# Kernel tuning notes

Hardware: AMD Instinct MI355X
Metric: run time of the kernel (lower is better)

## Reference

```python
import jax, jax.numpy as jnp
import numpy as np

TOP_K = 2


def setup_inputs() -> dict:
    key = jax.random.key(0)
    k1, k2 = jax.random.split(key)
    hidden_states = jax.random.normal(k1, (4, 8192, 4096), dtype=jnp.float32)
    weight = jax.random.normal(k2, (64, 4096), dtype=jnp.float32) * 0.02
    return {"hidden_states": hidden_states, "weight": weight}


def reference(hidden_states, weight):
    bsz, seq_len, h = hidden_states.shape
    x = hidden_states.reshape(-1, h)                      # [T, h]
    logits = jnp.einsum('th,eh->te', x, weight)           # [T, E] router logits
    scores = jax.nn.softmax(logits, axis=-1)
    topk_weight, topk_idx = jax.lax.top_k(scores, TOP_K)  # [T, k] each
    # norm_topk_prob is False in the module, so no renormalization.
    return topk_idx, topk_weight
```

## Files before the change

kernel.cpp:

```cpp
#include <hip/hip_runtime.h>
#include <math.h>


#define BK 64

__device__ __forceinline__ void gl_lds16(const float* g, float* l) {
  __builtin_amdgcn_global_load_lds(
      (const __attribute__((address_space(1))) unsigned int*)g,
      (__attribute__((address_space(3))) unsigned int*)l,
      16, 0, 0);
}

__global__ __launch_bounds__(256)
void moe_gate(const float* __restrict__ X, const float* __restrict__ W,
              float* __restrict__ out, int T) {
  __shared__ float smem[8192];
  float* sx = smem;
  float* sw = smem + 4096;

  const int t    = threadIdx.x;
  const int lane = t & 63;
  const int wave = t >> 6;
  const int tr   = t & 15;
  const int tc   = t >> 4;
  const long tok0 = (long)blockIdx.x * 64;

  const float* xg[4];
  const float* wg[4];
  float* ldx[4];
  float* ldw[4];
  {
    const int rl = lane >> 4;
    const int c4 = lane & 15;
    #pragma unroll
    for (int i = 0; i < 4; ++i) {
      const int r  = wave * 16 + i * 4 + rl;
      const int sz = (wave * 4 + i) & 15;
      const int gc = c4 ^ sz;
      xg[i] = X + (tok0 + r) * 4096 + gc * 4;
      wg[i] = W + (long)r * 4096 + gc * 4;
      ldx[i] = sx + (wave * 16 + i * 4) * 64;
      ldw[i] = sw + (wave * 16 + i * 4) * 64;
    }
  }

  float acc[4][4];
  #pragma unroll
  for (int i = 0; i < 4; ++i)
    #pragma unroll
    for (int j = 0; j < 4; ++j) acc[i][j] = 0.f;

  for (int k0 = 0; k0 < 4096; k0 += BK) {
    #pragma unroll
    for (int i = 0; i < 4; ++i) {
      gl_lds16(xg[i] + k0, ldx[i]);
      gl_lds16(wg[i] + k0, ldw[i]);
    }
    __syncthreads();

    float cacc[4][4];
    #pragma unroll
    for (int i = 0; i < 4; ++i)
      #pragma unroll
      for (int j = 0; j < 4; ++j) cacc[i][j] = 0.f;

    #pragma unroll
    for (int k4 = 0; k4 < 16; ++k4) {
      float4 xa[4], wb[4];
      #pragma unroll
      for (int i = 0; i < 4; ++i) {
        const int row  = tr * 4 + i;
        const int slot = k4 ^ (row >> 2);
        xa[i] = *(const float4*)(sx + row * 64 + slot * 4);
      }
      #pragma unroll
      for (int j = 0; j < 4; ++j) {
        const int e    = tc * 4 + j;
        const int slot = k4 ^ (e >> 2);
        wb[j] = *(const float4*)(sw + e * 64 + slot * 4);
      }
      #pragma unroll
      for (int i = 0; i < 4; ++i)
        #pragma unroll
        for (int j = 0; j < 4; ++j) {
          cacc[i][j] = fmaf(xa[i].x, wb[j].x, cacc[i][j]);
          cacc[i][j] = fmaf(xa[i].y, wb[j].y, cacc[i][j]);
          cacc[i][j] = fmaf(xa[i].z, wb[j].z, cacc[i][j]);
          cacc[i][j] = fmaf(xa[i].w, wb[j].w, cacc[i][j]);
        }
    }
    #pragma unroll
    for (int i = 0; i < 4; ++i)
      #pragma unroll
      for (int j = 0; j < 4; ++j) acc[i][j] += cacc[i][j];
    __syncthreads();
  }

  #pragma unroll
  for (int i = 0; i < 4; ++i)
    #pragma unroll
    for (int j = 0; j < 4; ++j)
      smem[(tr * 4 + i) * 65 + tc * 4 + j] = acc[i][j];
  __syncthreads();

  if (t < 64) {
    const float* row = smem + t * 65;
    float b1 = -1e30f, b2 = -1e30f;
    int i1 = 0, i2 = 0;
    for (int e = 0; e < 64; ++e) {
      const float v = row[e];
      if (v > b1)      { b2 = b1; i2 = i1; b1 = v; i1 = e; }
      else if (v > b2) { b2 = v; i2 = e; }
    }
    float s = 0.f;
    for (int e = 0; e < 64; ++e) s += expf(row[e] - b1);
    const float inv = 1.0f / s;
    const long gt = tok0 + t;
    out[gt * 2 + 0] = (float)i1;
    out[gt * 2 + 1] = (float)i2;
    float* ow = out + (long)T * 2;
    ow[gt * 2 + 0] = inv;
    ow[gt * 2 + 1] = expf(b2 - b1) * inv;
  }
}

extern "C" void kernel_launch(void* const* d_in, const int* in_sizes, int n_in,
                              void* d_out, int out_size, void* d_ws, size_t ws_size,
                              hipStream_t stream) {
  const float* X = (const float*)d_in[0];
  const float* W = (const float*)d_in[1];
  float* out = (float*)d_out;
  const int T = in_sizes[0] / 4096;
  const int grid = T / 64;
  hipLaunchKernelGGL(moe_gate, dim3(grid), dim3(256), 0, stream, X, W, out, T);
}
```

Baseline: 828.2 us.

## Restructure gate GEMM: per-lane token rows, wave-uniform expert weights, double-buffered X

The block grows to 512 threads, and each lane now owns one token and computes 8 experts. The expert index is made wave-uniform with readfirstlane, so W loads become scalar or broadcast reads straight from global memory instead of being staged in LDS. X is staged through a register-prefetched, double-buffered, XOR-swizzled LDS tile, which removes one sync per chunk and overlaps the next chunk's global load with compute. The trade-off is more registers per lane for 16 float4 X values, and W reads that depend on the scalar or cache path.

```diff
diff --git a/kernel.cpp b/kernel.cpp
--- a/kernel.cpp
+++ b/kernel.cpp
@@ -3,108 +3,87 @@
 
 
 #define BK 64
+#define NCHUNK (4096 / BK)
 
-__device__ __forceinline__ void gl_lds16(const float* g, float* l) {
-  __builtin_amdgcn_global_load_lds(
-      (const __attribute__((address_space(1))) unsigned int*)g,
-      (__attribute__((address_space(3))) unsigned int*)l,
-      16, 0, 0);
-}
-
-__global__ __launch_bounds__(256)
+__global__ __launch_bounds__(512, 4)
 void moe_gate(const float* __restrict__ X, const float* __restrict__ W,
               float* __restrict__ out, int T) {
-  __shared__ float smem[8192];
-  float* sx = smem;
-  float* sw = smem + 4096;
+  __shared__ float4 sx[2][1024];
+  __shared__ float slog[64 * 65];
 
   const int t    = threadIdx.x;
   const int lane = t & 63;
-  const int wave = t >> 6;
-  const int tr   = t & 15;
-  const int tc   = t >> 4;
+  const int e0   = __builtin_amdgcn_readfirstlane((t >> 6) << 3);
+
   const long tok0 = (long)blockIdx.x * 64;
 
-  const float* xg[4];
-  const float* wg[4];
-  float* ldx[4];
-  float* ldw[4];
+  const int srow0 = t >> 4;
+  const int srow1 = srow0 + 32;
+  const int sslot = t & 15;
+  const float* xsA = X + (tok0 + srow0) * 4096 + (sslot << 2);
+  const float* xsB = X + (tok0 + srow1) * 4096 + (sslot << 2);
+  const int dA = (srow0 << 8) + ((sslot ^ (srow0 & 15)) << 4);
+  const int dB = (srow1 << 8) + ((sslot ^ (srow1 & 15)) << 4);
+
+  const int xoff = (lane << 8) + ((lane & 15) << 4);
+
+  float acc[8];
+  #pragma unroll
+  for (int j = 0; j < 8; ++j) acc[j] = 0.f;
+
   {
-    const int rl = lane >> 4;
-    const int c4 = lane & 15;
+    float4 a = *(const float4*)xsA;
+    float4 b = *(const float4*)xsB;
+    *(float4*)((char*)(&sx[0][0]) + dA) = a;
+    *(float4*)((char*)(&sx[0][0]) + dB) = b;
+  }
+  __syncthreads();
+
+  for (int c = 0; c < NCHUNK; ++c) {
+    const int k0 = c * BK;
+    const char* xb = (const char*)(&sx[c & 1][0]);
+
+    float4 nA, nB;
+    if (c + 1 < NCHUNK) {
+      nA = *(const float4*)(xsA + k0 + BK);
+      nB = *(const float4*)(xsB + k0 + BK);
+    }
+
+    float4 xv[16];
     #pragma unroll
-    for (int i = 0; i < 4; ++i) {
-      const int r  = wave * 16 + i * 4 + rl;
-      const int sz = (wave * 4 + i) & 15;
-      const int gc = c4 ^ sz;
-      xg[i] = X + (tok0 + r) * 4096 + gc * 4;
-      wg[i] = W + (long)r * 4096 + gc * 4;
-      ldx[i] = sx + (wave * 16 + i * 4) * 64;
-      ldw[i] = sw + (wave * 16 + i * 4) * 64;
-    }
-  }
-
-  float acc[4][4];
-  #pragma unroll
-  for (int i = 0; i < 4; ++i)
-    #pragma unroll
-    for (int j = 0; j < 4; ++j) acc[i][j] = 0.f;
-
-  for (int k0 = 0; k0 < 4096; k0 += BK) {
-    #pragma unroll
-    for (int i = 0; i < 4; ++i) {
-      gl_lds16(xg[i] + k0, ldx[i]);
-      gl_lds16(wg[i] + k0, ldw[i]);
-    }
-    __syncthreads();
-
-    float cacc[4][4];
-    #pragma unroll
-    for (int i = 0; i < 4; ++i)
-      #pragma unroll
-      for (int j = 0; j < 4; ++j) cacc[i][j] = 0.f;
+    for (int g = 0; g < 16; ++g)
+      xv[g] = *(const float4*)(xb + (xoff ^ (g << 4)));
 
     #pragma unroll
-    for (int k4 = 0; k4 < 16; ++k4) {
-      float4 xa[4], wb[4];
+    for (int j = 0; j < 8; ++j) {
+      const float4* wq = (const float4*)(W + (long)(e0 + j) * 4096 + k0);
+      float c0 = 0.f, c1 = 0.f, c2 = 0.f, c3 = 0.f;
       #pragma unroll
-      for (int i = 0; i < 4; ++i) {
-        const int row  = tr * 4 + i;
-        const int slot = k4 ^ (row >> 2);
-        xa[i] = *(const float4*)(sx + row * 64 + slot * 4);
+      for (int g = 0; g < 16; ++g) {
+        const float4 wv = wq[g];
+        c0 = fmaf(xv[g].x, wv.x, c0);
+        c1 = fmaf(xv[g].y, wv.y, c1);
+        c2 = fmaf(xv[g].z, wv.z, c2);
+        c3 = fmaf(xv[g].w, wv.w, c3);
       }
-      #pragma unroll
-      for (int j = 0; j < 4; ++j) {
-        const int e    = tc * 4 + j;
-        const int slot = k4 ^ (e >> 2);
-        wb[j] = *(const float4*)(sw + e * 64 + slot * 4);
-      }
-      #pragma unroll
-      for (int i = 0; i < 4; ++i)
-        #pragma unroll
-        for (int j = 0; j < 4; ++j) {
-          cacc[i][j] = fmaf(xa[i].x, wb[j].x, cacc[i][j]);
-          cacc[i][j] = fmaf(xa[i].y, wb[j].y, cacc[i][j]);
-          cacc[i][j] = fmaf(xa[i].z, wb[j].z, cacc[i][j]);
-          cacc[i][j] = fmaf(xa[i].w, wb[j].w, cacc[i][j]);
-        }
+      acc[j] += (c0 + c1) + (c2 + c3);
     }
-    #pragma unroll
-    for (int i = 0; i < 4; ++i)
-      #pragma unroll
-      for (int j = 0; j < 4; ++j) acc[i][j] += cacc[i][j];
+
+    if (c + 1 < NCHUNK) {
+      char* xn = (char*)(&sx[(c + 1) & 1][0]);
+      *(float4*)(xn + dA) = nA;
+      *(float4*)(xn + dB) = nB;
+    }
     __syncthreads();
   }
 
   #pragma unroll
-  for (int i = 0; i < 4; ++i)
-    #pragma unroll
-    for (int j = 0; j < 4; ++j)
-      smem[(tr * 4 + i) * 65 + tc * 4 + j] = acc[i][j];
+  for (int j = 0; j < 8; ++j)
+    slog[lane * 65 + e0 + j] = acc[j];
   __syncthreads();
 
   if (t < 64) {
-    const float* row = smem + t * 65;
+    const float* row = slog + t * 65;
     float b1 = -1e30f, b2 = -1e30f;
     int i1 = 0, i2 = 0;
     for (int e = 0; e < 64; ++e) {
@@ -132,5 +111,5 @@
   float* out = (float*)d_out;
   const int T = in_sizes[0] / 4096;
   const int grid = T / 64;
-  hipLaunchKernelGGL(moe_gate, dim3(grid), dim3(256), 0, stream, X, W, out, T);
+  hipLaunchKernelGGL(moe_gate, dim3(grid), dim3(512), 0, stream, X, W, out, T);
 }
```

Measured after the change: 1.489 ms. 1.8x slower.
